# Kernel optimization log

Hardware: AMD Instinct MI355X
Metric: run time of the kernel (lower is better)

The kernel has to match this reference:

```python
import jax, jax.numpy as jnp
import numpy as np

B, S, D, H = 4, 1024, 768, 12
Dh = D // H
EPS = 1e-5


def _layer_norm(x, g, b):
    mu = jnp.mean(x, axis=-1, keepdims=True)
    var = jnp.var(x, axis=-1, keepdims=True)
    return (x - mu) * jax.lax.rsqrt(var + EPS) * g + b


def _mha(q_in, k_in, v_in, Wq, Wk, Wv, Wo, bias):
    # Wq/Wk/Wv: [H, D, Dh] (per-head projections, batched over heads)
    q = jnp.einsum('bsd,hdk->bhsk', q_in, Wq)
    k = jnp.einsum('btd,hdk->bhtk', k_in, Wk)
    v = jnp.einsum('btd,hdk->bhtk', v_in, Wv)
    w = jnp.einsum('bhsk,bhtk->bhst', q, k) * (Dh ** -0.5)
    a = jax.nn.softmax(w + bias, axis=-1)  # bias: 0 / -inf additive mask
    o = jnp.einsum('bhst,bhtk->bhsk', a, v)
    o = o.transpose(0, 2, 1, 3).reshape(q_in.shape[0], q_in.shape[1], H * Dh)  # concat heads
    return o @ Wo


def setup_inputs():
    key = jax.random.key(0)
    ks = jax.random.split(key, 16)
    s = 0.02
    inp = {
        'key_enc': jax.random.normal(ks[0], (B, S, D), jnp.float32),
        'value_enc': jax.random.normal(ks[1], (B, S, D), jnp.float32),
        'x': jax.random.normal(ks[2], (B, S, D), jnp.float32),
        'src_mask': jnp.ones((B, S), jnp.int32),
        'tgt_mask': jnp.ones((B, S), jnp.int32),
        'Wq_m': jax.random.normal(ks[3], (H, D, Dh), jnp.float32) * s,
        'Wk_m': jax.random.normal(ks[4], (H, D, Dh), jnp.float32) * s,
        'Wv_m': jax.random.normal(ks[5], (H, D, Dh), jnp.float32) * s,
        'Wo_m': jax.random.normal(ks[6], (D, D), jnp.float32) * s,
        'Wq_c': jax.random.normal(ks[7], (H, D, Dh), jnp.float32) * s,
        'Wk_c': jax.random.normal(ks[8], (H, D, Dh), jnp.float32) * s,
        'Wv_c': jax.random.normal(ks[9], (H, D, Dh), jnp.float32) * s,
        'Wo_c': jax.random.normal(ks[10], (D, D), jnp.float32) * s,
        'ln1_g': jnp.ones((D,), jnp.float32), 'ln1_b': jnp.zeros((D,), jnp.float32),
        'ln2_g': jnp.ones((D,), jnp.float32), 'ln2_b': jnp.zeros((D,), jnp.float32),
        'ln3_g': jnp.ones((D,), jnp.float32), 'ln3_b': jnp.zeros((D,), jnp.float32),
        'W1': jax.random.normal(ks[11], (D, 4 * D), jnp.float32) * s,
        'b1': jnp.zeros((4 * D,), jnp.float32),
        'W2': jax.random.normal(ks[12], (4 * D, D), jnp.float32) * s,
        'b2': jnp.zeros((D,), jnp.float32),
    }
    return inp


def reference(key_enc, value_enc, x, src_mask, tgt_mask,
              Wq_m, Wk_m, Wv_m, Wo_m, Wq_c, Wk_c, Wv_c, Wo_c,
              ln1_g, ln1_b, ln2_g, ln2_b, ln3_g, ln3_b, W1, b1, W2, b2):
    neg_inf = jnp.float32(-jnp.inf)
    causal = jnp.tril(jnp.ones((S, S), bool))
    # masked self-attn: causal AND target padding mask (mask broadcasts over query rows)
    allow_m = causal[None, None, :, :] & (tgt_mask[:, None, None, :] != 0)
    bias_m = jnp.where(allow_m, jnp.float32(0.0), neg_inf)
    h = _layer_norm(x + _mha(x, x, x, Wq_m, Wk_m, Wv_m, Wo_m, bias_m), ln1_g, ln1_b)
    # cross-attn: keys from `key_enc`, values from `value_enc`, queries from decoder stream
    allow_c = (src_mask[:, None, None, :] != 0)
    bias_c = jnp.where(allow_c, jnp.float32(0.0), neg_inf)
    h = _layer_norm(h + _mha(h, key_enc, value_enc, Wq_c, Wk_c, Wv_c, Wo_c, bias_c), ln2_g, ln2_b)
    # MLP with exact (erf) GELU, as torch nn.GELU default
    mlp = jax.nn.gelu(h @ W1 + b1, approximate=False) @ W2 + b2
    return _layer_norm(h + mlp, ln3_g, ln3_b)
```

## Files before the change

### kernel.cpp

```cpp
#include <hip/hip_runtime.h>
#include <math.h>

#define BB 4
#define SS 1024
#define DD 768
#define HH 12
#define DHD 64
#define MROWS 4096
#define FF 3072
#define WPC (DD * DD)

typedef unsigned short u16;
typedef float f32x4 __attribute__((ext_vector_type(4)));
typedef __bf16 bf16x8 __attribute__((ext_vector_type(8)));
typedef unsigned short u16x8 __attribute__((ext_vector_type(8)));
typedef unsigned short u16x4 __attribute__((ext_vector_type(4)));

static __device__ __forceinline__ float bf2f(u16 u) {
    union { unsigned int i; float f; } c; c.i = ((unsigned int)u) << 16; return c.f;
}
static __device__ __forceinline__ u16 f2bf(float f) {
    return __builtin_bit_cast(u16, static_cast<__bf16>(f));
}
static __device__ __forceinline__ int xcd_swz(int total) {
    const int bid = (int)blockIdx.x;
    return (bid & 7) * (total >> 3) + (bid >> 3);
}
static __device__ __forceinline__ void gload16(const u16* g, u16* l) {
    __builtin_amdgcn_global_load_lds(
        (const __attribute__((address_space(1))) void*)g,
        (__attribute__((address_space(3))) void*)l, 16, 0, 0);
}

static __device__ __forceinline__ void gemm128_core(
    const u16* __restrict__ A, const u16* __restrict__ Bt,
    int K,
    const float* __restrict__ bias, int do_gelu,
    u16* __restrict__ Cbf, int ldcbf, int cboff,
    int row0, int col0, u16* As0, u16* As1, u16* Bs0, u16* Bs1)
{
    const int tid  = threadIdx.x;
    const int lane = tid & 63;
    const int w    = tid >> 6;
    const int wm = (w >> 1) * 64;
    const int wn = (w & 1) * 64;

    const u16* Ap = A  + (size_t)(row0 + w * 32 + (lane >> 2)) * K + (lane & 3) * 8;
    const u16* Bp = Bt + (size_t)(col0 + w * 32 + (lane >> 2)) * K + (lane & 3) * 8;
    const int woff = (w * 32) * 32;

    const int fr = lane & 15;
    const int fk = (lane >> 4) * 8;
    const int afo = (wm + fr) * 32 + fk;
    const int bfo = (wn + fr) * 32 + fk;

    f32x4 acc[4][4] = {};

    for (int k0 = 0; k0 < K; k0 += 64) {
        if (k0) __syncthreads();
        gload16(Ap + k0,               As0 + woff);
        gload16(Ap + k0 + 16 * K,      As0 + woff + 16 * 32);
        gload16(Ap + k0 + 32,          As1 + woff);
        gload16(Ap + k0 + 32 + 16 * K, As1 + woff + 16 * 32);
        gload16(Bp + k0,               Bs0 + woff);
        gload16(Bp + k0 + 16 * K,      Bs0 + woff + 16 * 32);
        gload16(Bp + k0 + 32,          Bs1 + woff);
        gload16(Bp + k0 + 32 + 16 * K, Bs1 + woff + 16 * 32);
        __syncthreads();

        {
            bf16x8 af[4], bfv[4];
#pragma unroll
            for (int mi = 0; mi < 4; ++mi)
                af[mi] = __builtin_bit_cast(bf16x8,
                    *(const u16x8*)(As0 + afo + mi * 16 * 32));
#pragma unroll
            for (int ni = 0; ni < 4; ++ni)
                bfv[ni] = __builtin_bit_cast(bf16x8,
                    *(const u16x8*)(Bs0 + bfo + ni * 16 * 32));
#pragma unroll
            for (int mi = 0; mi < 4; ++mi)
#pragma unroll
                for (int ni = 0; ni < 4; ++ni)
                    acc[mi][ni] = __builtin_amdgcn_mfma_f32_16x16x32_bf16(
                        af[mi], bfv[ni], acc[mi][ni], 0, 0, 0);
        }
        {
            bf16x8 af[4], bfv[4];
#pragma unroll
            for (int mi = 0; mi < 4; ++mi)
                af[mi] = __builtin_bit_cast(bf16x8,
                    *(const u16x8*)(As1 + afo + mi * 16 * 32));
#pragma unroll
            for (int ni = 0; ni < 4; ++ni)
                bfv[ni] = __builtin_bit_cast(bf16x8,
                    *(const u16x8*)(Bs1 + bfo + ni * 16 * 32));
#pragma unroll
            for (int mi = 0; mi < 4; ++mi)
#pragma unroll
                for (int ni = 0; ni < 4; ++ni)
                    acc[mi][ni] = __builtin_amdgcn_mfma_f32_16x16x32_bf16(
                        af[mi], bfv[ni], acc[mi][ni], 0, 0, 0);
        }
    }

    const int orow0 = row0 + wm + (lane >> 4) * 4;
    const int ocol0 = col0 + wn + fr;
#pragma unroll
    for (int mi = 0; mi < 4; ++mi) {
#pragma unroll
        for (int ni = 0; ni < 4; ++ni) {
            const int col = ocol0 + ni * 16;
            const float bv = bias ? bias[col] : 0.0f;
#pragma unroll
            for (int r = 0; r < 4; ++r) {
                const int row = orow0 + mi * 16 + r;
                float v = acc[mi][ni][r] + bv;
                if (do_gelu) v = 0.5f * v * (1.0f + erff(v * 0.70710678118654752f));
                Cbf[(size_t)row * ldcbf + cboff + col] = f2bf(v);
            }
        }
    }
}

__global__ __launch_bounds__(256) void gemm128_mlp1(
    const u16* __restrict__ A, const u16* __restrict__ Bt,
    const float* __restrict__ bias, u16* __restrict__ Cbf)
{
    __shared__ u16 As0[128 * 32];
    __shared__ u16 As1[128 * 32];
    __shared__ u16 Bs0[128 * 32];
    __shared__ u16 Bs1[128 * 32];
    const int lid = xcd_swz(24 * 32);
    gemm128_core(A, Bt, DD, bias, 1, Cbf, FF, 0,
                 (lid / 24) * 128, (lid % 24) * 128, As0, As1, Bs0, Bs1);
}

__global__ __launch_bounds__(256) void gemm128_proj(
    const u16* __restrict__ BFx, const u16* __restrict__ BFK,
    const u16* __restrict__ BFV, const u16* __restrict__ Wm6,
    u16* __restrict__ QKV, u16* __restrict__ KVc)
{
    __shared__ u16 As0[128 * 32];
    __shared__ u16 As1[128 * 32];
    __shared__ u16 Bs0[128 * 32];
    __shared__ u16 Bs1[128 * 32];
    const int fid = xcd_swz(960);
    const u16* A; const u16* B; u16* C; int ldc, coff, row0, col0;
    if (fid < 576) {
        A = BFx; B = Wm6; C = QKV; ldc = 3 * DD; coff = 0;
        row0 = (fid / 18) * 128; col0 = (fid % 18) * 128;
    } else if (fid < 768) {
        const int l = fid - 576;
        A = BFK; B = Wm6 + 4 * WPC; C = KVc; ldc = 2 * DD; coff = 0;
        row0 = (l / 6) * 128; col0 = (l % 6) * 128;
    } else {
        const int l = fid - 768;
        A = BFV; B = Wm6 + 5 * WPC; C = KVc; ldc = 2 * DD; coff = DD;
        row0 = (l / 6) * 128; col0 = (l % 6) * 128;
    }
    gemm128_core(A, B, DD, nullptr, 0, C, ldc, coff, row0, col0,
                 As0, As1, Bs0, Bs1);
}

static __device__ __forceinline__ void gemm64_core(
    const u16* __restrict__ A, const u16* __restrict__ Bt,
    int N, int Kstride, int Klen,
    const float* __restrict__ bias,
    const float* __restrict__ residf, const u16* __restrict__ residb,
    u16* __restrict__ Cbf, int ldcbf, int cboff,
    int row0, int col0, u16* As0, u16* As1, u16* Bs0, u16* Bs1)
{
    const int tid  = threadIdx.x;
    const int lane = tid & 63;
    const int w    = tid >> 6;
    const int wm = (w >> 1) * 32;
    const int wn = (w & 1) * 64;

    const u16* Ap = A  + (size_t)(row0 + w * 16 + (lane >> 2)) * Kstride + (lane & 3) * 8;
    const u16* Bp = Bt + (size_t)(col0 + w * 32 + (lane >> 2)) * Kstride + (lane & 3) * 8;
    const int aoff = (w * 16) * 32;
    const int boff = (w * 32) * 32;

    const int fr = lane & 15;
    const int fk = (lane >> 4) * 8;
    const int afo = (wm + fr) * 32 + fk;
    const int bfo = (wn + fr) * 32 + fk;

    f32x4 acc[2][4] = {};

    for (int k0 = 0; k0 < Klen; k0 += 64) {
        if (k0) __syncthreads();
        gload16(Ap + k0,                     As0 + aoff);
        gload16(Ap + k0 + 32,                As1 + aoff);
        gload16(Bp + k0,                     Bs0 + boff);
        gload16(Bp + k0 + 16 * Kstride,      Bs0 + boff + 16 * 32);
        gload16(Bp + k0 + 32,                Bs1 + boff);
        gload16(Bp + k0 + 32 + 16 * Kstride, Bs1 + boff + 16 * 32);
        __syncthreads();

        {
            bf16x8 af[2], bfv[4];
#pragma unroll
            for (int mi = 0; mi < 2; ++mi)
                af[mi] = __builtin_bit_cast(bf16x8,
                    *(const u16x8*)(As0 + afo + mi * 16 * 32));
#pragma unroll
            for (int ni = 0; ni < 4; ++ni)
                bfv[ni] = __builtin_bit_cast(bf16x8,
                    *(const u16x8*)(Bs0 + bfo + ni * 16 * 32));
#pragma unroll
            for (int mi = 0; mi < 2; ++mi)
#pragma unroll
                for (int ni = 0; ni < 4; ++ni)
                    acc[mi][ni] = __builtin_amdgcn_mfma_f32_16x16x32_bf16(
                        af[mi], bfv[ni], acc[mi][ni], 0, 0, 0);
        }
        {
            bf16x8 af[2], bfv[4];
#pragma unroll
            for (int mi = 0; mi < 2; ++mi)
                af[mi] = __builtin_bit_cast(bf16x8,
                    *(const u16x8*)(As1 + afo + mi * 16 * 32));
#pragma unroll
            for (int ni = 0; ni < 4; ++ni)
                bfv[ni] = __builtin_bit_cast(bf16x8,
                    *(const u16x8*)(Bs1 + bfo + ni * 16 * 32));
#pragma unroll
            for (int mi = 0; mi < 2; ++mi)
#pragma unroll
                for (int ni = 0; ni < 4; ++ni)
                    acc[mi][ni] = __builtin_amdgcn_mfma_f32_16x16x32_bf16(
                        af[mi], bfv[ni], acc[mi][ni], 0, 0, 0);
        }
    }

    const int orow0 = row0 + wm + (lane >> 4) * 4;
    const int ocol0 = col0 + wn + fr;
#pragma unroll
    for (int mi = 0; mi < 2; ++mi) {
#pragma unroll
        for (int ni = 0; ni < 4; ++ni) {
            const int col = ocol0 + ni * 16;
            const float bv = bias ? bias[col] : 0.0f;
#pragma unroll
            for (int r = 0; r < 4; ++r) {
                const int row = orow0 + mi * 16 + r;
                float v = acc[mi][ni][r] + bv;
                if (residf) v += residf[(size_t)row * N + col];
                if (residb) v += bf2f(residb[(size_t)row * N + col]);
                Cbf[(size_t)row * ldcbf + cboff + col] = f2bf(v);
            }
        }
    }
}

__global__ __launch_bounds__(256) void gemm64(
    const u16* __restrict__ A, const u16* __restrict__ Bt, int K,
    const float* __restrict__ residf, const u16* __restrict__ residb,
    u16* __restrict__ Cbf, int ldcbf)
{
    __shared__ u16 As0[64 * 32];
    __shared__ u16 As1[64 * 32];
    __shared__ u16 Bs0[128 * 32];
    __shared__ u16 Bs1[128 * 32];
    const int lid = xcd_swz(6 * 64);
    gemm64_core(A, Bt, DD, K, K, nullptr, residf, residb, Cbf, ldcbf, 0,
                (lid / 6) * 64, (lid % 6) * 128, As0, As1, Bs0, Bs1);
}

__global__ __launch_bounds__(256) void gemm64_sk(
    const u16* __restrict__ A, const u16* __restrict__ Bt,
    u16* __restrict__ Cpair)
{
    __shared__ u16 As0[64 * 32];
    __shared__ u16 As1[64 * 32];
    __shared__ u16 Bs0[128 * 32];
    __shared__ u16 Bs1[128 * 32];
    const int lid = xcd_swz(6 * 64 * 2);
    const int x = lid % 6;
    const int rem = lid / 6;
    const int y = rem % 64;
    const int z = rem / 64;
    const int koff = z * (FF / 2);
    gemm64_core(A + koff, Bt + koff, DD, FF, FF / 2,
                nullptr, nullptr, nullptr,
                Cpair + (size_t)z * MROWS * DD, DD, 0,
                y * 64, x * 128, As0, As1, Bs0, Bs1);
}

static __device__ __forceinline__ void tcvt_body(
    const float* __restrict__ in, u16* __restrict__ out,
    int K, int N, int bx, int by)
{
    __shared__ float t[32][33];
    const int n0 = bx * 32, k0 = by * 32;
    const int tx = threadIdx.x & 31, ty = threadIdx.x >> 5;
#pragma unroll
    for (int j = 0; j < 4; ++j)
        t[ty + j * 8][tx] = in[(size_t)(k0 + ty + j * 8) * N + n0 + tx];
    __syncthreads();
#pragma unroll
    for (int j = 0; j < 4; ++j)
        out[(size_t)(n0 + ty + j * 8) * K + k0 + tx] = f2bf(t[tx][ty + j * 8]);
}

__global__ __launch_bounds__(256) void prep_all(
    const float* __restrict__ x, const float* __restrict__ key_enc,
    const float* __restrict__ value_enc,
    u16* __restrict__ BFx, u16* __restrict__ BFK, u16* __restrict__ BFV,
    const float* __restrict__ wq_m, const float* __restrict__ wk_m,
    const float* __restrict__ wv_m, const float* __restrict__ wq_c,
    const float* __restrict__ wk_c, const float* __restrict__ wv_c,
    u16* __restrict__ Wm6,
    const float* __restrict__ wom, const float* __restrict__ woc,
    const float* __restrict__ w1, const float* __restrict__ w2,
    u16* __restrict__ womt, u16* __restrict__ woct,
    u16* __restrict__ w1t, u16* __restrict__ w2t)
{
    const int fid = (int)blockIdx.x;
    const int tid = threadIdx.x;
    if (fid < 9216) {
        const int z = fid / 3072;
        const float* s = (z == 0) ? x : (z == 1) ? key_enc : value_enc;
        u16* d = (z == 0) ? BFx : (z == 1) ? BFK : BFV;
        const int i = (fid % 3072) * 256 + tid;
        float4 v = ((const float4*)s)[i];
        ushort4 o;
        o.x = f2bf(v.x); o.y = f2bf(v.y); o.z = f2bf(v.z); o.w = f2bf(v.w);
        ((ushort4*)d)[i] = o;
    } else if (fid < 12672) {
        const int l = fid - 9216;
        const int z = l / 48;
        const int r = l % 48;
        const int wi = z / 12, head = z % 12;
        const float* wsel = (wi == 0) ? wq_m : (wi == 1) ? wk_m :
                            (wi == 2) ? wv_m : (wi == 3) ? wq_c :
                            (wi == 4) ? wk_c : wv_c;
        const float* ib = wsel + (size_t)head * DD * DHD;
        u16* ob = Wm6 + (size_t)wi * WPC + (size_t)head * DHD * DD;
        __shared__ float t[32][33];
        const int n0 = (r % 2) * 32, k0 = (r / 2) * 32;
        const int tx = tid & 31, ty = tid >> 5;
#pragma unroll
        for (int j = 0; j < 4; ++j)
            t[ty + j * 8][tx] = ib[(size_t)(k0 + ty + j * 8) * DHD + n0 + tx];
        __syncthreads();
#pragma unroll
        for (int j = 0; j < 4; ++j)
            ob[(size_t)(n0 + ty + j * 8) * DD + k0 + tx] = f2bf(t[tx][ty + j * 8]);
    } else {
        const int l = fid - 12672;
        if (l < 576) {
            tcvt_body(wom, womt, DD, DD, l % 24, l / 24);
        } else if (l < 1152) {
            const int m = l - 576;
            tcvt_body(woc, woct, DD, DD, m % 24, m / 24);
        } else if (l < 3456) {
            const int m = l - 1152;
            tcvt_body(w1, w1t, DD, FF, m % 96, m / 96);
        } else {
            const int m = l - 3456;
            tcvt_body(w2, w2t, FF, DD, m % 24, m / 24);
        }
    }
}

#define KAST 72
#define PAST 136
#define CSC 0.18033688011112042f
__global__ __launch_bounds__(256) void attn_mfma_kernel(
    const u16* __restrict__ Q, int ldq,
    const u16* __restrict__ K, const u16* __restrict__ V, int ldkv,
    const int* __restrict__ kmask, u16* __restrict__ O, int causal)
{
    const int lid = xcd_swz(16 * BB * HH);
    const int qtl = lid % 16;
    const int bh  = lid / 16;
    const int qt = causal ? (15 - qtl) : qtl;
    const int b  = bh / HH;
    const int h  = bh % HH;
    const int tid  = threadIdx.x;
    const int lane = tid & 63;
    const int w    = tid >> 6;
    const int lr = lane & 15;
    const int lg = lane >> 4;

    __shared__ u16 Ks[128 * KAST];
    __shared__ u16 Ps[64 * PAST];
    __shared__ u16 Vt[64 * PAST];

    const int row0 = qt * 64;
    const int q0w  = row0 + w * 16;

    bf16x8 qf[2];
    {
        const u16* qp = Q + (size_t)(b * SS + q0w + lr) * ldq + h * DHD + lg * 8;
        qf[0] = __builtin_bit_cast(bf16x8, *(const u16x8*)(qp));
        qf[1] = __builtin_bit_cast(bf16x8, *(const u16x8*)(qp + 32));
    }

    const int sr  = tid >> 1;
    const int scb = (tid & 1) * 32;
    const int vk  = tid >> 1;
    const int vdb = (tid & 1) * 32;
    const int k6  = vk & 63;
    const int vcol = ((vk >> 6) << 6) | ((k6 & 15) << 2) | (k6 >> 4);

    f32x4 acc[4] = {};
    float lsum[4] = {0.0f, 0.0f, 0.0f, 0.0f};

    const int nkt = causal ? ((qt + 2) >> 1) : 8;

    u16x8 kr0, kr1, kr2, kr3, vr0, vr1, vr2, vr3;
    {
        const u16* kp = K + (size_t)(b * SS + sr) * ldkv + h * DHD + scb;
        kr0 = *(const u16x8*)(kp);
        kr1 = *(const u16x8*)(kp + 8);
        kr2 = *(const u16x8*)(kp + 16);
        kr3 = *(const u16x8*)(kp + 24);
        const u16* vp = V + (size_t)(b * SS + vk) * ldkv + h * DHD + vdb;
        vr0 = *(const u16x8*)(vp);
        vr1 = *(const u16x8*)(vp + 8);
        vr2 = *(const u16x8*)(vp + 16);
        vr3 = *(const u16x8*)(vp + 24);
    }

    for (int kt = 0; kt < nkt; ++kt) {
        const int kcol0 = kt * 128;
        if (kt) __syncthreads();

        *(u16x8*)(&Ks[sr * KAST + scb])      = kr0;
        *(u16x8*)(&Ks[sr * KAST + scb + 8])  = kr1;
        *(u16x8*)(&Ks[sr * KAST + scb + 16]) = kr2;
        *(u16x8*)(&Ks[sr * KAST + scb + 24]) = kr3;
#pragma unroll
        for (int j = 0; j < 8; ++j) Vt[(vdb + j) * PAST + vcol]      = vr0[j];
#pragma unroll
        for (int j = 0; j < 8; ++j) Vt[(vdb + 8 + j) * PAST + vcol]  = vr1[j];
#pragma unroll
        for (int j = 0; j < 8; ++j) Vt[(vdb + 16 + j) * PAST + vcol] = vr2[j];
#pragma unroll
        for (int j = 0; j < 8; ++j) Vt[(vdb + 24 + j) * PAST + vcol] = vr3[j];
        __syncthreads();

        if (kt + 1 < nkt) {
            const int kn = kcol0 + 128;
            const u16* kp = K + (size_t)(b * SS + kn + sr) * ldkv + h * DHD + scb;
            kr0 = *(const u16x8*)(kp);
            kr1 = *(const u16x8*)(kp + 8);
            kr2 = *(const u16x8*)(kp + 16);
            kr3 = *(const u16x8*)(kp + 24);
            const u16* vp = V + (size_t)(b * SS + kn + vk) * ldkv + h * DHD + vdb;
            vr0 = *(const u16x8*)(vp);
            vr1 = *(const u16x8*)(vp + 8);
            vr2 = *(const u16x8*)(vp + 16);
            vr3 = *(const u16x8*)(vp + 24);
        }

        f32x4 s[8] = {};
        __builtin_amdgcn_s_setprio(1);
#pragma unroll
        for (int fi = 0; fi < 8; ++fi) {
            bf16x8 kf0 = __builtin_bit_cast(bf16x8, *(const u16x8*)(&Ks[(fi * 16 + lr) * KAST + lg * 8]));
            bf16x8 kf1 = __builtin_bit_cast(bf16x8, *(const u16x8*)(&Ks[(fi * 16 + lr) * KAST + 32 + lg * 8]));
            s[fi] = __builtin_amdgcn_mfma_f32_16x16x32_bf16(qf[0], kf0, s[fi], 0, 0, 0);
            s[fi] = __builtin_amdgcn_mfma_f32_16x16x32_bf16(qf[1], kf1, s[fi], 0, 0, 0);
        }
        __builtin_amdgcn_s_setprio(0);

        float biasf[8];
#pragma unroll
        for (int fi = 0; fi < 8; ++fi)
            biasf[fi] = kmask[b * SS + kcol0 + fi * 16 + lr] ? 0.0f : -INFINITY;
        const bool diag = (causal != 0) && (kt == nkt - 1);

#pragma unroll
        for (int r = 0; r < 4; ++r) {
            const int qrow = q0w + lg * 4 + r;
            const int prow = (w * 16 + lg * 4 + r) * PAST;
            u16x4 pk0, pk1;
            float rs = 0.0f;
#pragma unroll
            for (int fi = 0; fi < 8; ++fi) {
                float v = fmaf(s[fi][r], CSC, biasf[fi]);
                if (diag) {
                    const int key = kcol0 + fi * 16 + lr;
                    v = (key <= qrow) ? v : -INFINITY;
                }
                const float pv = exp2f(v);
                if (fi < 4) pk0[fi] = f2bf(pv); else pk1[fi - 4] = f2bf(pv);
                rs += pv;
            }
            lsum[r] += rs;
            *(u16x4*)(&Ps[prow + lr * 4])      = pk0;
            *(u16x4*)(&Ps[prow + 64 + lr * 4]) = pk1;
        }

        __builtin_amdgcn_s_setprio(1);
#pragma unroll
        for (int kk = 0; kk < 4; ++kk) {
            bf16x8 pf = __builtin_bit_cast(bf16x8, *(const u16x8*)(&Ps[(w * 16 + lr) * PAST + kk * 32 + lg * 8]));
#pragma unroll
            for (int di = 0; di < 4; ++di) {
                bf16x8 vf = __builtin_bit_cast(bf16x8, *(const u16x8*)(&Vt[(di * 16 + lr) * PAST + kk * 32 + lg * 8]));
                acc[di] = __builtin_amdgcn_mfma_f32_16x16x32_bf16(pf, vf, acc[di], 0, 0, 0);
            }
        }
        __builtin_amdgcn_s_setprio(0);
    }

#pragma unroll
    for (int r = 0; r < 4; ++r) {
        float l = lsum[r];
        l += __shfl_xor(l, 1);
        l += __shfl_xor(l, 2);
        l += __shfl_xor(l, 4);
        l += __shfl_xor(l, 8);
        const float inv = (l > 0.0f) ? (1.0f / l) : 0.0f;
        const size_t orow = (size_t)(b * SS + q0w + lg * 4 + r) * DD + h * DHD;
#pragma unroll
        for (int di = 0; di < 4; ++di)
            O[orow + di * 16 + lr] = f2bf(acc[di][r] * inv);
    }
}

__global__ __launch_bounds__(256) void ln_bf_kernel(
    const u16* __restrict__ X, const float* __restrict__ gma,
    const float* __restrict__ bta, u16* __restrict__ Ybf)
{
    const int row = blockIdx.x;
    const int tid = threadIdx.x;
    const u16* x = X + (size_t)row * DD;

    const float v0 = bf2f(x[tid]);
    const float v1 = bf2f(x[tid + 256]);
    const float v2 = bf2f(x[tid + 512]);

    __shared__ float sd[256];
    sd[tid] = v0 + v1 + v2;
    __syncthreads();
    for (int off = 128; off > 0; off >>= 1) {
        if (tid < off) sd[tid] += sd[tid + off];
        __syncthreads();
    }
    const float mean = sd[0] * (1.0f / 768.0f);
    __syncthreads();

    const float q0 = v0 - mean, q1 = v1 - mean, q2 = v2 - mean;
    sd[tid] = q0 * q0 + q1 * q1 + q2 * q2;
    __syncthreads();
    for (int off = 128; off > 0; off >>= 1) {
        if (tid < off) sd[tid] += sd[tid + off];
        __syncthreads();
    }
    const float var = sd[0] * (1.0f / 768.0f);
    const float inv = rsqrtf(var + 1e-5f);

    u16* yb = Ybf + (size_t)row * DD;
    yb[tid]       = f2bf(q0 * inv * gma[tid]       + bta[tid]);
    yb[tid + 256] = f2bf(q1 * inv * gma[tid + 256] + bta[tid + 256]);
    yb[tid + 512] = f2bf(q2 * inv * gma[tid + 512] + bta[tid + 512]);
}

__global__ __launch_bounds__(256) void ln_red_kernel(
    const u16* __restrict__ P0, const u16* __restrict__ P1,
    const float* __restrict__ bias, const u16* __restrict__ resid,
    const float* __restrict__ gma, const float* __restrict__ bta,
    float* __restrict__ Y)
{
    const int row = blockIdx.x;
    const int tid = threadIdx.x;
    const size_t base = (size_t)row * DD;

    float v[3];
#pragma unroll
    for (int j = 0; j < 3; ++j) {
        const int i = tid + j * 256;
        v[j] = bf2f(P0[base + i]) + bf2f(P1[base + i]) + bias[i] + bf2f(resid[base + i]);
    }

    __shared__ float sd[256];
    sd[tid] = v[0] + v[1] + v[2];
    __syncthreads();
    for (int off = 128; off > 0; off >>= 1) {
        if (tid < off) sd[tid] += sd[tid + off];
        __syncthreads();
    }
    const float mean = sd[0] * (1.0f / 768.0f);
    __syncthreads();

    float q[3];
#pragma unroll
    for (int j = 0; j < 3; ++j) q[j] = v[j] - mean;
    sd[tid] = q[0] * q[0] + q[1] * q[1] + q[2] * q[2];
    __syncthreads();
    for (int off = 128; off > 0; off >>= 1) {
        if (tid < off) sd[tid] += sd[tid + off];
        __syncthreads();
    }
    const float var = sd[0] * (1.0f / 768.0f);
    const float inv = rsqrtf(var + 1e-5f);

    float* y = Y + base;
#pragma unroll
    for (int j = 0; j < 3; ++j) {
        const int i = tid + j * 256;
        y[i] = q[j] * inv * gma[i] + bta[i];
    }
}

extern "C" void kernel_launch(void* const* d_in, const int* in_sizes, int n_in,
                              void* d_out, int out_size, void* d_ws, size_t ws_size,
                              hipStream_t stream)
{
    (void)in_sizes; (void)n_in; (void)out_size; (void)ws_size;

    const float* key_enc   = (const float*)d_in[0];
    const float* value_enc = (const float*)d_in[1];
    const float* x         = (const float*)d_in[2];
    const int*   src_mask  = (const int*)d_in[3];
    const int*   tgt_mask  = (const int*)d_in[4];
    const float* Wq_m = (const float*)d_in[5];
    const float* Wk_m = (const float*)d_in[6];
    const float* Wv_m = (const float*)d_in[7];
    const float* Wo_m = (const float*)d_in[8];
    const float* Wq_c = (const float*)d_in[9];
    const float* Wk_c = (const float*)d_in[10];
    const float* Wv_c = (const float*)d_in[11];
    const float* Wo_c = (const float*)d_in[12];
    const float* ln1_g = (const float*)d_in[13];
    const float* ln1_b = (const float*)d_in[14];
    const float* ln2_g = (const float*)d_in[15];
    const float* ln2_b = (const float*)d_in[16];
    const float* ln3_g = (const float*)d_in[17];
    const float* ln3_b = (const float*)d_in[18];
    const float* W1 = (const float*)d_in[19];
    const float* b1 = (const float*)d_in[20];
    const float* W2 = (const float*)d_in[21];
    const float* b2 = (const float*)d_in[22];

    float* out = (float*)d_out;

    const size_t ACT = (size_t)MROWS * DD;
    char* p = (char*)d_ws;
    u16* QKV  = (u16*)p;   p += 3 * ACT * 2;
    u16* BFx  = (u16*)p;   p += ACT * 2;
    u16* BFK  = (u16*)p;   p += ACT * 2;
    u16* BFV  = (u16*)p;   p += ACT * 2;
    u16* BF1a = (u16*)p;   p += ACT * 2;
    u16* BF1h = (u16*)p;   p += ACT * 2;
    u16* T2bf = (u16*)p;   p += ACT * 2;
    u16* SKKV = (u16*)p;   p += 2 * ACT * 2;
    u16* Wm6  = (u16*)p;   p += 6 * (size_t)WPC * 2;
    u16* Wom_t = (u16*)p;  p += (size_t)WPC * 2;
    u16* Woc_t = (u16*)p;  p += (size_t)WPC * 2;
    u16* W1t  = (u16*)p;   p += (size_t)DD * FF * 2;
    u16* W2t  = (u16*)p;   p += (size_t)DD * FF * 2;
    u16* MID  = QKV;
    u16* KVc  = SKKV;
    u16* SK0  = SKKV;
    u16* SK1  = SKKV + ACT;

    const dim3 blk(256);

    prep_all<<<dim3(18432), blk, 0, stream>>>(
        x, key_enc, value_enc, BFx, BFK, BFV,
        Wq_m, Wk_m, Wv_m, Wq_c, Wk_c, Wv_c, Wm6,
        Wo_m, Wo_c, W1, W2, Wom_t, Woc_t, W1t, W2t);

    gemm128_proj<<<dim3(960), blk, 0, stream>>>(BFx, BFK, BFV, Wm6, QKV, KVc);

    attn_mfma_kernel<<<dim3(768), blk, 0, stream>>>(
        QKV, 3 * DD, QKV + DD, QKV + 2 * DD, 3 * DD, tgt_mask, BF1a, 1);
    gemm64<<<dim3(384), blk, 0, stream>>>(BF1a, Wom_t, DD,
                                          x, nullptr, T2bf, DD);
    ln_bf_kernel<<<MROWS, blk, 0, stream>>>(T2bf, ln1_g, ln1_b, BF1h);

    gemm64<<<dim3(384), blk, 0, stream>>>(BF1h, Wm6 + 3 * WPC, DD,
                                          nullptr, nullptr, QKV, 3 * DD);
    attn_mfma_kernel<<<dim3(768), blk, 0, stream>>>(
        QKV, 3 * DD, KVc, KVc + DD, 2 * DD, src_mask, BF1a, 0);
    gemm64<<<dim3(384), blk, 0, stream>>>(BF1a, Woc_t, DD,
                                          nullptr, BF1h, T2bf, DD);
    ln_bf_kernel<<<MROWS, blk, 0, stream>>>(T2bf, ln2_g, ln2_b, BF1h);

    gemm128_mlp1<<<dim3(768), blk, 0, stream>>>(BF1h, W1t, b1, MID);
    gemm64_sk<<<dim3(768), blk, 0, stream>>>(MID, W2t, SKKV);
    ln_red_kernel<<<MROWS, blk, 0, stream>>>(SK0, SK1, b2, BF1h,
                                             ln3_g, ln3_b, out);
}
```

Measured before the change: 260.4 us.

## Split-K the attention output projections and use a cheaper sigmoid-form GELU

Both attention output-projection GEMMs now use the split-K kernel with two K halves, giving 768 blocks instead of 384. The two partial results are summed in a generalized LayerNorm-reduce kernel that also adds the residual, so the old GEMM epilogue residual add and the separate LN kernels go away. The exact erf GELU in the MLP1 epilogue is replaced by a tanh-style approximation computed with exp2 and a hardware reciprocal, which is cheaper but changes numerics slightly. Split-K adds partial-sum writes and reads in exchange for better use of the compute units.

```diff
diff --git a/kernel.cpp b/kernel.cpp
--- a/kernel.cpp
+++ b/kernel.cpp
@@ -30,6 +30,11 @@
     __builtin_amdgcn_global_load_lds(
         (const __attribute__((address_space(1))) void*)g,
         (__attribute__((address_space(3))) void*)l, 16, 0, 0);
+}
+static __device__ __forceinline__ float gelu_f(float x) {
+    const float x2 = x * x;
+    const float t  = x * fmaf(x2, -0.10294437f, -2.30220800f);
+    return x * __builtin_amdgcn_rcpf(1.0f + exp2f(t));
 }
 
 static __device__ __forceinline__ void gemm128_core(
@@ -116,7 +121,7 @@
             for (int r = 0; r < 4; ++r) {
                 const int row = orow0 + mi * 16 + r;
                 float v = acc[mi][ni][r] + bv;
-                if (do_gelu) v = 0.5f * v * (1.0f + erff(v * 0.70710678118654752f));
+                if (do_gelu) v = gelu_f(v);
                 Cbf[(size_t)row * ldcbf + cboff + col] = f2bf(v);
             }
         }
@@ -166,8 +171,6 @@
 static __device__ __forceinline__ void gemm64_core(
     const u16* __restrict__ A, const u16* __restrict__ Bt,
     int N, int Kstride, int Klen,
-    const float* __restrict__ bias,
-    const float* __restrict__ residf, const u16* __restrict__ residb,
     u16* __restrict__ Cbf, int ldcbf, int cboff,
     int row0, int col0, u16* As0, u16* As1, u16* Bs0, u16* Bs1)
 {
@@ -242,22 +245,17 @@
 #pragma unroll
         for (int ni = 0; ni < 4; ++ni) {
             const int col = ocol0 + ni * 16;
-            const float bv = bias ? bias[col] : 0.0f;
 #pragma unroll
             for (int r = 0; r < 4; ++r) {
                 const int row = orow0 + mi * 16 + r;
-                float v = acc[mi][ni][r] + bv;
-                if (residf) v += residf[(size_t)row * N + col];
-                if (residb) v += bf2f(residb[(size_t)row * N + col]);
-                Cbf[(size_t)row * ldcbf + cboff + col] = f2bf(v);
+                Cbf[(size_t)row * ldcbf + cboff + col] = f2bf(acc[mi][ni][r]);
             }
         }
     }
 }
 
 __global__ __launch_bounds__(256) void gemm64(
-    const u16* __restrict__ A, const u16* __restrict__ Bt, int K,
-    const float* __restrict__ residf, const u16* __restrict__ residb,
+    const u16* __restrict__ A, const u16* __restrict__ Bt,
     u16* __restrict__ Cbf, int ldcbf)
 {
     __shared__ u16 As0[64 * 32];
@@ -265,13 +263,13 @@
     __shared__ u16 Bs0[128 * 32];
     __shared__ u16 Bs1[128 * 32];
     const int lid = xcd_swz(6 * 64);
-    gemm64_core(A, Bt, DD, K, K, nullptr, residf, residb, Cbf, ldcbf, 0,
+    gemm64_core(A, Bt, DD, DD, DD, Cbf, ldcbf, 0,
                 (lid / 6) * 64, (lid % 6) * 128, As0, As1, Bs0, Bs1);
 }
 
 __global__ __launch_bounds__(256) void gemm64_sk(
     const u16* __restrict__ A, const u16* __restrict__ Bt,
-    u16* __restrict__ Cpair)
+    int Kstride, int Khalf, u16* __restrict__ Cpair)
 {
     __shared__ u16 As0[64 * 32];
     __shared__ u16 As1[64 * 32];
@@ -282,9 +280,8 @@
     const int rem = lid / 6;
     const int y = rem % 64;
     const int z = rem / 64;
-    const int koff = z * (FF / 2);
-    gemm64_core(A + koff, Bt + koff, DD, FF, FF / 2,
-                nullptr, nullptr, nullptr,
+    const int koff = z * Khalf;
+    gemm64_core(A + koff, Bt + koff, DD, Kstride, Khalf,
                 Cpair + (size_t)z * MROWS * DD, DD, 0,
                 y * 64, x * 128, As0, As1, Bs0, Bs1);
 }
@@ -525,49 +522,12 @@
     }
 }
 
-__global__ __launch_bounds__(256) void ln_bf_kernel(
-    const u16* __restrict__ X, const float* __restrict__ gma,
-    const float* __restrict__ bta, u16* __restrict__ Ybf)
-{
-    const int row = blockIdx.x;
-    const int tid = threadIdx.x;
-    const u16* x = X + (size_t)row * DD;
-
-    const float v0 = bf2f(x[tid]);
-    const float v1 = bf2f(x[tid + 256]);
-    const float v2 = bf2f(x[tid + 512]);
-
-    __shared__ float sd[256];
-    sd[tid] = v0 + v1 + v2;
-    __syncthreads();
-    for (int off = 128; off > 0; off >>= 1) {
-        if (tid < off) sd[tid] += sd[tid + off];
-        __syncthreads();
-    }
-    const float mean = sd[0] * (1.0f / 768.0f);
-    __syncthreads();
-
-    const float q0 = v0 - mean, q1 = v1 - mean, q2 = v2 - mean;
-    sd[tid] = q0 * q0 + q1 * q1 + q2 * q2;
-    __syncthreads();
-    for (int off = 128; off > 0; off >>= 1) {
-        if (tid < off) sd[tid] += sd[tid + off];
-        __syncthreads();
-    }
-    const float var = sd[0] * (1.0f / 768.0f);
-    const float inv = rsqrtf(var + 1e-5f);
-
-    u16* yb = Ybf + (size_t)row * DD;
-    yb[tid]       = f2bf(q0 * inv * gma[tid]       + bta[tid]);
-    yb[tid + 256] = f2bf(q1 * inv * gma[tid + 256] + bta[tid + 256]);
-    yb[tid + 512] = f2bf(q2 * inv * gma[tid + 512] + bta[tid + 512]);
-}
-
-__global__ __launch_bounds__(256) void ln_red_kernel(
+__global__ __launch_bounds__(256) void ln_red_gen(
     const u16* __restrict__ P0, const u16* __restrict__ P1,
-    const float* __restrict__ bias, const u16* __restrict__ resid,
+    const float* __restrict__ bias,
+    const float* __restrict__ residf, const u16* __restrict__ residb,
     const float* __restrict__ gma, const float* __restrict__ bta,
-    float* __restrict__ Y)
+    float* __restrict__ Yf, u16* __restrict__ Ybf)
 {
     const int row = blockIdx.x;
     const int tid = threadIdx.x;
@@ -577,7 +537,11 @@
 #pragma unroll
     for (int j = 0; j < 3; ++j) {
         const int i = tid + j * 256;
-        v[j] = bf2f(P0[base + i]) + bf2f(P1[base + i]) + bias[i] + bf2f(resid[base + i]);
+        float t = bf2f(P0[base + i]) + bf2f(P1[base + i]);
+        if (bias)   t += bias[i];
+        if (residf) t += residf[base + i];
+        if (residb) t += bf2f(residb[base + i]);
+        v[j] = t;
     }
 
     __shared__ float sd[256];
@@ -602,11 +566,12 @@
     const float var = sd[0] * (1.0f / 768.0f);
     const float inv = rsqrtf(var + 1e-5f);
 
-    float* y = Y + base;
 #pragma unroll
     for (int j = 0; j < 3; ++j) {
         const int i = tid + j * 256;
-        y[i] = q[j] * inv * gma[i] + bta[i];
+        const float y = q[j] * inv * gma[i] + bta[i];
+        if (Yf)  Yf[base + i] = y;
+        if (Ybf) Ybf[base + i] = f2bf(y);
     }
 }
 
@@ -659,8 +624,11 @@
     u16* W2t  = (u16*)p;   p += (size_t)DD * FF * 2;
     u16* MID  = QKV;
     u16* KVc  = SKKV;
+    u16* SKa  = QKV;
+    u16* SKb  = QKV + ACT;
     u16* SK0  = SKKV;
     u16* SK1  = SKKV + ACT;
+    (void)T2bf;
 
     const dim3 blk(256);
 
@@ -673,20 +641,19 @@
 
     attn_mfma_kernel<<<dim3(768), blk, 0, stream>>>(
         QKV, 3 * DD, QKV + DD, QKV + 2 * DD, 3 * DD, tgt_mask, BF1a, 1);
-    gemm64<<<dim3(384), blk, 0, stream>>>(BF1a, Wom_t, DD,
-                                          x, nullptr, T2bf, DD);
-    ln_bf_kernel<<<MROWS, blk, 0, stream>>>(T2bf, ln1_g, ln1_b, BF1h);
-
-    gemm64<<<dim3(384), blk, 0, stream>>>(BF1h, Wm6 + 3 * WPC, DD,
-                                          nullptr, nullptr, QKV, 3 * DD);
+    gemm64_sk<<<dim3(768), blk, 0, stream>>>(BF1a, Wom_t, DD, DD / 2, SKa);
+    ln_red_gen<<<MROWS, blk, 0, stream>>>(SKa, SKb, nullptr, x, nullptr,
+                                          ln1_g, ln1_b, nullptr, BF1h);
+
+    gemm64<<<dim3(384), blk, 0, stream>>>(BF1h, Wm6 + 3 * WPC, QKV, 3 * DD);
     attn_mfma_kernel<<<dim3(768), blk, 0, stream>>>(
         QKV, 3 * DD, KVc, KVc + DD, 2 * DD, src_mask, BF1a, 0);
-    gemm64<<<dim3(384), blk, 0, stream>>>(BF1a, Woc_t, DD,
-                                          nullptr, BF1h, T2bf, DD);
-    ln_bf_kernel<<<MROWS, blk, 0, stream>>>(T2bf, ln2_g, ln2_b, BF1h);
+    gemm64_sk<<<dim3(768), blk, 0, stream>>>(BF1a, Woc_t, DD, DD / 2, SKa);
+    ln_red_gen<<<MROWS, blk, 0, stream>>>(SKa, SKb, nullptr, nullptr, BF1h,
+                                          ln2_g, ln2_b, nullptr, BF1h);
 
     gemm128_mlp1<<<dim3(768), blk, 0, stream>>>(BF1h, W1t, b1, MID);
-    gemm64_sk<<<dim3(768), blk, 0, stream>>>(MID, W2t, SKKV);
-    ln_red_kernel<<<MROWS, blk, 0, stream>>>(SK0, SK1, b2, BF1h,
-                                             ln3_g, ln3_b, out);
-}
+    gemm64_sk<<<dim3(768), blk, 0, stream>>>(MID, W2t, FF, FF / 2, SK0);
+    ln_red_gen<<<MROWS, blk, 0, stream>>>(SK0, SK1, b2, nullptr, BF1h,
+                                          ln3_g, ln3_b, out, nullptr);
+}
```

Result: faster. 253.0 us (-2.8%).
